# Kernel tuning notes

Measured on AMD Instinct MI355X. Metric: run time of the kernel, lower is better.

## Reference

```python
import jax, jax.numpy as jnp
import numpy as np

B, M, G = 4096, 4096, 16384

def setup_inputs() -> dict:
    key = jax.random.key(0)
    k1, k2, k3, k4 = jax.random.split(key, 4)
    x = jax.random.uniform(k1, (B, M), dtype=jnp.float32)  # probabilistic bits in [0,1]
    idx_l = jax.random.randint(k2, (G,), 0, M, dtype=jnp.int64)
    idx_r = jax.random.randint(k3, (G,), 0, M, dtype=jnp.int64)
    alpha = 0.01 * jax.random.normal(k4, (G, 3), dtype=jnp.float32)  # [G, K=3] logits
    return {"x": x, "idx_l": idx_l, "idx_r": idx_r, "alpha": alpha}

def reference(x, idx_l, idx_r, alpha):
    # Gather the two inputs of each gate: a, b are [B, G]
    a = x[:, idx_l]
    b = x[:, idx_r]
    ab = a * b
    # Soft gate probabilities over {AND, OR, XOR}: w is [G, 3]
    w = jax.nn.softmax(alpha, axis=-1)
    # AND = a*b ; OR = a + b - a*b ; XOR = a + b - 2*a*b
    s = a + b
    y = w[:, 0] * ab + w[:, 1] * (s - ab) + w[:, 2] * (s - 2.0 * ab)
    return y  # [B, G]
```

## Files before the change

kernel.cpp:

```cpp
#include <hip/hip_runtime.h>
#include <hip/hip_bf16.h>


#define B_DIM 4096
#define M_DIM 4096
#define G_DIM 16384

__global__ __launch_bounds__(256) void prep_gates(
    const int* __restrict__ idx_l, const int* __restrict__ idx_r,
    const float* __restrict__ alpha, int4* __restrict__ gates, int G)
{
    int g = blockIdx.x * blockDim.x + threadIdx.x;
    if (g >= G) return;
    float a0 = alpha[g * 3 + 0];
    float a1 = alpha[g * 3 + 1];
    float a2 = alpha[g * 3 + 2];
    float m  = fmaxf(a0, fmaxf(a1, a2));
    float e0 = expf(a0 - m);
    float e1 = expf(a1 - m);
    float e2 = expf(a2 - m);
    float inv = 1.0f / (e0 + e1 + e2);
    float w0 = e0 * inv, w1 = e1 * inv, w2 = e2 * inv;
    float c0 = w0 - w1 - 2.0f * w2;
    float c1 = w1 + w2;
    int4 rec;
    rec.x = idx_l[g];
    rec.y = idx_r[g];
    rec.z = __float_as_int(c0);
    rec.w = __float_as_int(c1);
    gates[g] = rec;
}

__global__ __launch_bounds__(256) void gate_main(
    const float* __restrict__ x, const int4* __restrict__ gates,
    float* __restrict__ out, int M, int G)
{
    __shared__ float row[M_DIM];

    const int b = blockIdx.x;
    const float* xrow = x + (size_t)b * M;

    const float4* xr4  = reinterpret_cast<const float4*>(xrow);
    float4*       row4 = reinterpret_cast<float4*>(row);
    #pragma unroll
    for (int i = 0; i < M_DIM / 4 / 256; ++i) {
        row4[threadIdx.x + i * 256] = xr4[threadIdx.x + i * 256];
    }
    __syncthreads();

    float* orow = out + (size_t)b * G;

    for (int g4 = threadIdx.x; g4 < G / 4; g4 += 256) {
        const int g = g4 * 4;
        float4 y;
        float* yp = &y.x;
        #pragma unroll
        for (int k = 0; k < 4; ++k) {
            int4 rec = gates[g + k];
            float a  = row[rec.x];
            float bb = row[rec.y];
            float c0 = __int_as_float(rec.z);
            float c1 = __int_as_float(rec.w);
            yp[k] = c0 * (a * bb) + c1 * (a + bb);
        }
        reinterpret_cast<float4*>(orow)[g4] = y;
    }
}

extern "C" void kernel_launch(void* const* d_in, const int* in_sizes, int n_in,
                              void* d_out, int out_size, void* d_ws, size_t ws_size,
                              hipStream_t stream)
{
    const float* x     = (const float*)d_in[0];
    const int*   idx_l = (const int*)d_in[1];
    const int*   idx_r = (const int*)d_in[2];
    const float* alpha = (const float*)d_in[3];
    float*       out   = (float*)d_out;

    int4* gates = (int4*)d_ws;

    prep_gates<<<(G_DIM + 255) / 256, 256, 0, stream>>>(idx_l, idx_r, alpha, gates, G_DIM);
    gate_main<<<B_DIM, 256, 0, stream>>>(x, gates, out, M_DIM, G_DIM);
}
```

Measured before the change: 374.9 us.

## Process two batch rows per block to reuse gate records across rows

Each block now loads two rows of x into shared memory and reuses each gate record for both rows. This halves the global reads of the gate table per output element. Stores change from float4 per thread over four gates to scalar coalesced stores, one gate per thread per row. The larger shared-memory footprint (32KB) may reduce occupancy, and there are half as many blocks.

```diff
diff --git a/kernel.cpp b/kernel.cpp
--- a/kernel.cpp
+++ b/kernel.cpp
@@ -5,6 +5,7 @@
 #define B_DIM 4096
 #define M_DIM 4096
 #define G_DIM 16384
+#define ROWS  2
 
 __global__ __launch_bounds__(256) void prep_gates(
     const int* __restrict__ idx_l, const int* __restrict__ idx_r,
@@ -33,37 +34,34 @@
 
 __global__ __launch_bounds__(256) void gate_main(
     const float* __restrict__ x, const int4* __restrict__ gates,
-    float* __restrict__ out, int M, int G)
+    float* __restrict__ out)
 {
-    __shared__ float row[M_DIM];
+    __shared__ float rows[ROWS * M_DIM];
 
-    const int b = blockIdx.x;
-    const float* xrow = x + (size_t)b * M;
+    const int b0 = blockIdx.x * ROWS;
+    const float* xbase = x + (size_t)b0 * M_DIM;
 
-    const float4* xr4  = reinterpret_cast<const float4*>(xrow);
-    float4*       row4 = reinterpret_cast<float4*>(row);
+    const float4* xr4   = reinterpret_cast<const float4*>(xbase);
+    float4*       rows4 = reinterpret_cast<float4*>(rows);
     #pragma unroll
-    for (int i = 0; i < M_DIM / 4 / 256; ++i) {
-        row4[threadIdx.x + i * 256] = xr4[threadIdx.x + i * 256];
+    for (int i = 0; i < ROWS * M_DIM / 4 / 256; ++i) {
+        rows4[threadIdx.x + i * 256] = xr4[threadIdx.x + i * 256];
     }
     __syncthreads();
 
-    float* orow = out + (size_t)b * G;
+    float* o0 = out + (size_t)b0 * G_DIM;
 
-    for (int g4 = threadIdx.x; g4 < G / 4; g4 += 256) {
-        const int g = g4 * 4;
-        float4 y;
-        float* yp = &y.x;
+    #pragma unroll 4
+    for (int g = threadIdx.x; g < G_DIM; g += 256) {
+        int4 rec = gates[g];
+        float c0 = __int_as_float(rec.z);
+        float c1 = __int_as_float(rec.w);
         #pragma unroll
-        for (int k = 0; k < 4; ++k) {
-            int4 rec = gates[g + k];
-            float a  = row[rec.x];
-            float bb = row[rec.y];
-            float c0 = __int_as_float(rec.z);
-            float c1 = __int_as_float(rec.w);
-            yp[k] = c0 * (a * bb) + c1 * (a + bb);
+        for (int r = 0; r < ROWS; ++r) {
+            float a  = rows[r * M_DIM + rec.x];
+            float bb = rows[r * M_DIM + rec.y];
+            o0[(size_t)r * G_DIM + g] = c0 * (a * bb) + c1 * (a + bb);
         }
-        reinterpret_cast<float4*>(orow)[g4] = y;
     }
 }
 
@@ -80,5 +78,5 @@
     int4* gates = (int4*)d_ws;
 
     prep_gates<<<(G_DIM + 255) / 256, 256, 0, stream>>>(idx_l, idx_r, alpha, gates, G_DIM);
-    gate_main<<<B_DIM, 256, 0, stream>>>(x, gates, out, M_DIM, G_DIM);
+    gate_main<<<B_DIM / ROWS, 256, 0, stream>>>(x, gates, out);
 }
```

Result: faster. 332.7 us (-11.2%).
